# Performance work log

Measured on AMD Instinct MI355X. Metric: run time of the kernel, lower is better.

## Reference

```python
import jax, jax.numpy as jnp
import numpy as np

B, S, HID = 2, 1024, 2048
NH, NKV = 32, 8
HD = HID // NH          # 64
N_REP = NH // NKV       # 4
ROPE_BASE = 10000.0


def rope_tables(seq_len, dim):
    inv_freq = 1.0 / (ROPE_BASE ** (np.arange(0, dim, 2, dtype=np.float32) / dim))
    t = jnp.arange(seq_len, dtype=jnp.float32)
    freqs = jnp.outer(t, jnp.asarray(inv_freq))          # [S, HD/2]
    emb = jnp.concatenate([freqs, freqs], axis=-1)       # [S, HD]
    return jnp.cos(emb), jnp.sin(emb)


def rotate_half(x):
    half = x.shape[-1] // 2
    return jnp.concatenate([-x[..., half:], x[..., :half]], axis=-1)


def setup_inputs() -> dict:
    key = jax.random.key(0)
    k1, k2, k3, k4, k5 = jax.random.split(key, 5)
    hidden_states = jax.random.normal(k1, (B, S, HID), dtype=jnp.float32)
    position_ids = jnp.broadcast_to(jnp.arange(S, dtype=jnp.int32), (B, S))
    # additive causal mask [B,1,S,S]: 0 where allowed, large negative where masked
    neg = jnp.finfo(jnp.float32).min
    causal = jnp.tril(jnp.ones((S, S), dtype=bool))
    attention_mask = jnp.where(causal, 0.0, neg)[None, None].astype(jnp.float32)
    attention_mask = jnp.broadcast_to(attention_mask, (B, 1, S, S))
    scale = 0.02
    Wq = jax.random.normal(k2, (HID, NH * HD), dtype=jnp.float32) * scale
    Wk = jax.random.normal(k3, (HID, NKV * HD), dtype=jnp.float32) * scale
    Wv = jax.random.normal(k4, (HID, NKV * HD), dtype=jnp.float32) * scale
    Wo = jax.random.normal(k5, (HID, HID), dtype=jnp.float32) * scale
    return {"hidden_states": hidden_states, "position_ids": position_ids,
            "attention_mask": attention_mask, "Wq": Wq, "Wk": Wk, "Wv": Wv, "Wo": Wo}


def reference(hidden_states, position_ids, attention_mask, Wq, Wk, Wv, Wo):
    b, s, _ = hidden_states.shape
    q = (hidden_states @ Wq).reshape(b, s, NH, HD).transpose(0, 2, 1, 3)    # [b,H,s,d]
    k = (hidden_states @ Wk).reshape(b, s, NKV, HD).transpose(0, 2, 1, 3)   # [b,kv,s,d]
    v = (hidden_states @ Wv).reshape(b, s, NKV, HD).transpose(0, 2, 1, 3)

    cos_t, sin_t = rope_tables(s, HD)                    # [s, d]
    cos = cos_t[position_ids][:, None]                   # [b,1,s,d]
    sin = sin_t[position_ids][:, None]
    q = q * cos + rotate_half(q) * sin
    k = k * cos + rotate_half(k) * sin

    # GQA: repeat each kv head N_REP times along the head axis
    k = jnp.repeat(k, N_REP, axis=1)                     # [b,H,s,d]
    v = jnp.repeat(v, N_REP, axis=1)

    scale = 1.0 / jnp.sqrt(jnp.asarray(HD, dtype=q.dtype))
    scores = jnp.einsum('bhqd,bhkd->bhqk', q, k) * scale
    scores = scores + attention_mask
    scores = jnp.maximum(scores, jnp.finfo(scores.dtype).min)
    w = jax.nn.softmax(scores, axis=-1)
    out = jnp.einsum('bhqk,bhkd->bhqd', w, v)            # [b,H,s,d]
    out = out.transpose(0, 2, 1, 3).reshape(b, s, HID)
    return out @ Wo
```

## Files before the change

kernel.cpp:

```cpp
#include <hip/hip_runtime.h>
#include <hip/hip_bf16.h>
#include <math.h>

constexpr int BB   = 2;
constexpr int SS   = 1024;
constexpr int HID  = 2048;
constexpr int NH   = 32;
constexpr int NKV  = 8;
constexpr int HD   = 64;
constexpr int M    = BB * SS;
constexpr int NQKV = 3072;

typedef __attribute__((ext_vector_type(8))) short bf8v;
typedef __attribute__((ext_vector_type(4))) float f4v;

static __device__ __forceinline__ unsigned short f2b(float x) {
  __hip_bfloat16 h = __float2bfloat16(x);
  return *reinterpret_cast<unsigned short*>(&h);
}
static __device__ __forceinline__ void gload16(void* lds, const void* g) {
  __builtin_amdgcn_global_load_lds(
      (const __attribute__((address_space(1))) void*)g,
      (__attribute__((address_space(3))) void*)lds, 16, 0, 0);
}

__global__ __launch_bounds__(256) void prepAll(
    const float* __restrict__ Wq, const float* __restrict__ Wk,
    const float* __restrict__ Wv, const float* __restrict__ Wo,
    const float* __restrict__ hidden, const int* __restrict__ pos_ids,
    unsigned short* __restrict__ WqkvT, unsigned short* __restrict__ WoT,
    unsigned short* __restrict__ Xb, float2* __restrict__ tab) {
  const int z = blockIdx.z;
  const int t = threadIdx.x;

  if (z == 4) {
    const int idx = blockIdx.y * 32 + blockIdx.x;
    if ((t & 127) < 32) {
      const int m = idx * 2 + (t >> 7);
      const int j = t & 31;
      const float pos = (float)pos_ids[m];
      const float ang = pos * exp2f(-(float)j * (13.287712379549449f / 32.0f));
      float sn, cs;
      sincosf(ang, &sn, &cs);
      tab[(size_t)m * 32 + j] = make_float2(cs, sn);
    }
    return;
  }
  if (z == 5) {
    const size_t base = ((size_t)(blockIdx.y * 32 + blockIdx.x)) * 4096;
#pragma unroll
    for (int it = 0; it < 2; ++it) {
      const size_t i = base + it * 2048 + t * 8;
      const float4 v0 = *(const float4*)(hidden + i);
      const float4 v1 = *(const float4*)(hidden + i + 4);
      unsigned short o[8] = {f2b(v0.x), f2b(v0.y), f2b(v0.z), f2b(v0.w),
                             f2b(v1.x), f2b(v1.y), f2b(v1.z), f2b(v1.w)};
      *(bf8v*)(Xb + i) = *(bf8v*)o;
    }
    return;
  }

  const float* src;
  unsigned short* dst;
  int C;
  if (z == 0)      { src = Wq; dst = WqkvT;                      C = 2048; }
  else if (z == 1) { src = Wk; dst = WqkvT + (size_t)2048 * HID; C = 512;  }
  else if (z == 2) { src = Wv; dst = WqkvT + (size_t)2560 * HID; C = 512;  }
  else             { src = Wo; dst = WoT;                        C = 2048; }

  const int r0 = blockIdx.y * 64, c0 = blockIdx.x * 64;
  if (c0 >= C) return;
  __shared__ float T[64][65];
  {
    const int r  = t >> 2;
    const int c4 = (t & 3) * 16;
    const float* sp = src + (size_t)(r0 + r) * C + c0 + c4;
    *(float4*)&T[r][c4 + 0]  = *(const float4*)(sp + 0);
    *(float4*)&T[r][c4 + 4]  = *(const float4*)(sp + 4);
    *(float4*)&T[r][c4 + 8]  = *(const float4*)(sp + 8);
    *(float4*)&T[r][c4 + 12] = *(const float4*)(sp + 12);
  }
  __syncthreads();
  {
    const int c  = t >> 2;
    const int rr = (t & 3) * 16;
    unsigned short o[16];
#pragma unroll
    for (int i = 0; i < 16; ++i) o[i] = f2b(T[rr + i][c]);
    unsigned short* dp = dst + (size_t)(c0 + c) * HID + r0 + rr;
    *(bf8v*)dp       = *(bf8v*)&o[0];
    *(bf8v*)(dp + 8) = *(bf8v*)&o[8];
  }
}


__global__ __launch_bounds__(256) void gemm_qkv(
    const unsigned short* __restrict__ A, const unsigned short* __restrict__ Bt,
    const float2* __restrict__ tab,
    unsigned short* __restrict__ Qb, unsigned short* __restrict__ Kb,
    unsigned short* __restrict__ Vt) {
  __shared__ unsigned short As[4][64 * 32];
  __shared__ unsigned short Bs[4][128 * 32];
  const int t  = threadIdx.x;
  const int w  = t >> 6, l = t & 63;
  const int lr = l & 15, lg = l >> 4;
  const int wr = w >> 1, wc = w & 1;
  const int bm = blockIdx.y * 64, bn = blockIdx.x * 128;

  f4v acc[2][4] = {};

  const unsigned short* Ablk = A  + (size_t)bm * HID;
  const unsigned short* Bblk = Bt + (size_t)bn * HID;
  const int srow = l >> 2;
  const int scol = (((l & 3) ^ ((srow >> 1) & 3)) * 8);
  const int rsl  = (lg ^ ((lr >> 1) & 3)) * 8;

  auto stage = [&](int buf, int k0) {
    gload16(&As[buf][(w * 16) * 32], Ablk + (size_t)(w * 16 + srow) * HID + k0 + scol);
    gload16(&Bs[buf][(w * 32)      * 32], Bblk + (size_t)(w * 32 +      srow) * HID + k0 + scol);
    gload16(&Bs[buf][(w * 32 + 16) * 32], Bblk + (size_t)(w * 32 + 16 + srow) * HID + k0 + scol);
  };

  const int nsteps = HID / 32;
  stage(0, 0);
  stage(1, 32);
  stage(2, 64);
  asm volatile("s_waitcnt vmcnt(6)" ::: "memory");
  __builtin_amdgcn_s_barrier();

  const int aoff = (wr * 32 + lr) * 32 + rsl;
  const int boff = (wc * 64 + lr) * 32 + rsl;
  for (int tt = 0; tt < nsteps; ++tt) {
    const int cur = tt & 3;
    if (tt + 3 < nsteps) stage((tt + 3) & 3, (tt + 3) * 32);

    bf8v aF[2], bF[4];
#pragma unroll
    for (int i = 0; i < 2; ++i)
      aF[i] = *(const bf8v*)&As[cur][aoff + i * 512];
#pragma unroll
    for (int j = 0; j < 4; ++j)
      bF[j] = *(const bf8v*)&Bs[cur][boff + j * 512];
    __builtin_amdgcn_s_setprio(1);
#pragma unroll
    for (int mi = 0; mi < 2; ++mi)
#pragma unroll
      for (int ni = 0; ni < 4; ++ni)
        acc[mi][ni] = __builtin_amdgcn_mfma_f32_16x16x32_bf16(aF[mi], bF[ni], acc[mi][ni], 0, 0, 0);
    __builtin_amdgcn_s_setprio(0);

    if (tt + 3 < nsteps)      { asm volatile("s_waitcnt vmcnt(6)" ::: "memory"); }
    else if (tt + 2 < nsteps) { asm volatile("s_waitcnt vmcnt(3)" ::: "memory"); }
    else                      { asm volatile("s_waitcnt vmcnt(0)" ::: "memory"); }
    __builtin_amdgcn_s_barrier();
  }

  const int row0 = bm + wr * 32;
  const int colHead = bn + wc * 64;
  int mode, hh;
  if (colHead < 2048)      { mode = 0; hh = colHead >> 6;          }
  else if (colHead < 2560) { mode = 1; hh = (colHead - 2048) >> 6; }
  else                     { mode = 2; hh = (colHead - 2560) >> 6; }

#pragma unroll
  for (int mi = 0; mi < 2; ++mi)
#pragma unroll
    for (int r = 0; r < 4; ++r) {
      const int rowg = row0 + mi * 16 + lg * 4 + r;
      const int bI = rowg >> 10, s = rowg & (SS - 1);
      if (mode == 2) {
        unsigned short* base = Vt + ((size_t)(bI * NKV + hh) * 64) * SS + s;
#pragma unroll
        for (int ni = 0; ni < 4; ++ni)
          base[(size_t)(ni * 16 + lr) * SS] = f2b(acc[mi][ni][r]);
      } else {
        unsigned short* dst = (mode == 0)
            ? Qb + ((size_t)(bI * NH  + hh) * SS + s) * 64
            : Kb + ((size_t)(bI * NKV + hh) * SS + s) * 64;
        const float2 cs_lo = tab[(size_t)rowg * 32 + lr];
        const float2 cs_hi = tab[(size_t)rowg * 32 + 16 + lr];
#pragma unroll
        for (int ni = 0; ni < 4; ++ni) {
          const float2 cs = (ni & 1) ? cs_hi : cs_lo;
          const float x   = acc[mi][ni][r];
          const float prt = acc[mi][ni ^ 2][r];
          const float rh  = (ni < 2) ? -prt : prt;
          float v = x * cs.x + rh * cs.y;
          if (mode == 0) v *= 0.125f;
          dst[ni * 16 + lr] = f2b(v);
        }
      }
    }
}

__global__ __launch_bounds__(256) void gemm_bf16(
    const unsigned short* __restrict__ A, const unsigned short* __restrict__ Bt,
    float* __restrict__ C, int Ndim) {
  __shared__ unsigned short As[4][64 * 32];
  __shared__ unsigned short Bs[4][128 * 32];
  const int t  = threadIdx.x;
  const int w  = t >> 6, l = t & 63;
  const int lr = l & 15, lg = l >> 4;
  const int wr = w >> 1, wc = w & 1;
  const int bm = blockIdx.y * 64, bn = blockIdx.x * 128;

  f4v acc[2][4] = {};

  const unsigned short* Ablk = A  + (size_t)bm * HID;
  const unsigned short* Bblk = Bt + (size_t)bn * HID;
  const int srow = l >> 2;
  const int scol = (((l & 3) ^ ((srow >> 1) & 3)) * 8);
  const int rsl  = (lg ^ ((lr >> 1) & 3)) * 8;

  auto stage = [&](int buf, int k0) {
    gload16(&As[buf][(w * 16) * 32], Ablk + (size_t)(w * 16 + srow) * HID + k0 + scol);
    gload16(&Bs[buf][(w * 32)      * 32], Bblk + (size_t)(w * 32 +      srow) * HID + k0 + scol);
    gload16(&Bs[buf][(w * 32 + 16) * 32], Bblk + (size_t)(w * 32 + 16 + srow) * HID + k0 + scol);
  };

  const int nsteps = HID / 32;
  stage(0, 0);
  stage(1, 32);
  stage(2, 64);
  asm volatile("s_waitcnt vmcnt(6)" ::: "memory");
  __builtin_amdgcn_s_barrier();

  const int aoff = (wr * 32 + lr) * 32 + rsl;
  const int boff = (wc * 64 + lr) * 32 + rsl;
  for (int tt = 0; tt < nsteps; ++tt) {
    const int cur = tt & 3;
    if (tt + 3 < nsteps) stage((tt + 3) & 3, (tt + 3) * 32);

    bf8v aF[2], bF[4];
#pragma unroll
    for (int i = 0; i < 2; ++i)
      aF[i] = *(const bf8v*)&As[cur][aoff + i * 512];
#pragma unroll
    for (int j = 0; j < 4; ++j)
      bF[j] = *(const bf8v*)&Bs[cur][boff + j * 512];
    __builtin_amdgcn_s_setprio(1);
#pragma unroll
    for (int mi = 0; mi < 2; ++mi)
#pragma unroll
      for (int ni = 0; ni < 4; ++ni)
        acc[mi][ni] = __builtin_amdgcn_mfma_f32_16x16x32_bf16(aF[mi], bF[ni], acc[mi][ni], 0, 0, 0);
    __builtin_amdgcn_s_setprio(0);

    if (tt + 3 < nsteps)      { asm volatile("s_waitcnt vmcnt(6)" ::: "memory"); }
    else if (tt + 2 < nsteps) { asm volatile("s_waitcnt vmcnt(3)" ::: "memory"); }
    else                      { asm volatile("s_waitcnt vmcnt(0)" ::: "memory"); }
    __builtin_amdgcn_s_barrier();
  }

  const int row0 = bm + wr * 32;
  const int col0 = bn + wc * 64;
#pragma unroll
  for (int mi = 0; mi < 2; ++mi)
#pragma unroll
    for (int r = 0; r < 4; ++r) {
      const size_t rowoff = (size_t)(row0 + mi * 16 + lg * 4 + r) * Ndim;
#pragma unroll
      for (int ni = 0; ni < 4; ++ni)
        C[rowoff + col0 + ni * 16 + lr] = acc[mi][ni][r];
    }
}

__global__ __launch_bounds__(128) void attn_mfma(
    const unsigned short* __restrict__ Qb, const unsigned short* __restrict__ Kb,
    const unsigned short* __restrict__ Vt, unsigned short* __restrict__ attn) {
  const int xb = blockIdx.x;
  const int h = blockIdx.y, b = blockIdx.z;
  const int kv = h >> 2;
  const int w  = threadIdx.x >> 6;
  const int l  = threadIdx.x & 63;
  const int lr = l & 15;
  const int lg = l >> 4;
  const int t  = threadIdx.x;

  __shared__ unsigned short VT[64][72];
  __shared__ unsigned short PL[2][16][72];

  const unsigned short* Kp = Kb + ((size_t)((b * NKV + kv) * SS)) * 64;
  const unsigned short* Vp = Vt + ((size_t)((b * NKV + kv) * 64)) * SS;

  const int vd  = t >> 1;
  const int vso = (t & 1) * 32;

  for (int half = 0; half < 2; ++half) {
    const int qt = half ? (31 - xb) : xb;
    const int qbase = qt * 32;
    const int qW = qbase + w * 16;
    const unsigned short* Qp = Qb + ((size_t)((b * NH + h) * SS + qW)) * 64;
    bf8v aQ0 = *(const bf8v*)(Qp + (size_t)lr * 64 + lg * 8);
    bf8v aQ1 = *(const bf8v*)(Qp + (size_t)lr * 64 + 32 + lg * 8);

    f4v o[4] = {{0,0,0,0},{0,0,0,0},{0,0,0,0},{0,0,0,0}};
    float lsumL[4] = {0.f, 0.f, 0.f, 0.f};

    bf8v kc[8];
#pragma unroll
    for (int c = 0; c < 4; ++c) {
      const unsigned short* kr = Kp + (size_t)(c * 16 + lr) * 64 + lg * 8;
      kc[2 * c]     = *(const bf8v*)(kr);
      kc[2 * c + 1] = *(const bf8v*)(kr + 32);
    }

    for (int kvb = 0; kvb < qbase + 32; kvb += 64) {
      __syncthreads();
      const unsigned short* vp = Vp + (size_t)vd * SS + kvb + vso;
      const bf8v v0 = *(const bf8v*)(vp);
      const bf8v v1 = *(const bf8v*)(vp + 8);
      const bf8v v2 = *(const bf8v*)(vp + 16);
      const bf8v v3 = *(const bf8v*)(vp + 24);

      f4v sc[4] = {{0,0,0,0},{0,0,0,0},{0,0,0,0},{0,0,0,0}};
      __builtin_amdgcn_s_setprio(1);
#pragma unroll
      for (int c = 0; c < 4; ++c) {
        sc[c] = __builtin_amdgcn_mfma_f32_16x16x32_bf16(aQ0, kc[2 * c],     sc[c], 0, 0, 0);
        sc[c] = __builtin_amdgcn_mfma_f32_16x16x32_bf16(aQ1, kc[2 * c + 1], sc[c], 0, 0, 0);
      }
      __builtin_amdgcn_s_setprio(0);

      if (kvb + 64 < qbase + 32) {
#pragma unroll
        for (int c = 0; c < 4; ++c) {
          const unsigned short* kr = Kp + (size_t)(kvb + 64 + c * 16 + lr) * 64 + lg * 8;
          kc[2 * c]     = *(const bf8v*)(kr);
          kc[2 * c + 1] = *(const bf8v*)(kr + 32);
        }
      }

#pragma unroll
      for (int r = 0; r < 4; ++r) {
        const int qrow = qW + lg * 4 + r;
        float ps = 0.f;
        unsigned short pb[4];
#pragma unroll
        for (int c = 0; c < 4; ++c) {
          const float s = ((kvb + c * 16 + lr) > qrow) ? -INFINITY : sc[c][r];
          const float p = __expf(s);
          ps += p;
          pb[c] = f2b(p);
        }
        lsumL[r] += ps;
#pragma unroll
        for (int c = 0; c < 4; ++c) PL[w][lg * 4 + r][c * 16 + lr] = pb[c];
      }

      *(bf8v*)&VT[vd][vso]      = v0;
      *(bf8v*)&VT[vd][vso + 8]  = v1;
      *(bf8v*)&VT[vd][vso + 16] = v2;
      *(bf8v*)&VT[vd][vso + 24] = v3;

      __syncthreads();

      bf8v aP0 = *(const bf8v*)&PL[w][lr][lg * 8];
      bf8v aP1 = *(const bf8v*)&PL[w][lr][32 + lg * 8];
      __builtin_amdgcn_s_setprio(1);
#pragma unroll
      for (int n = 0; n < 4; ++n) {
        bf8v bV0 = *(const bf8v*)&VT[n * 16 + lr][lg * 8];
        bf8v bV1 = *(const bf8v*)&VT[n * 16 + lr][32 + lg * 8];
        o[n] = __builtin_amdgcn_mfma_f32_16x16x32_bf16(aP0, bV0, o[n], 0, 0, 0);
        o[n] = __builtin_amdgcn_mfma_f32_16x16x32_bf16(aP1, bV1, o[n], 0, 0, 0);
      }
      __builtin_amdgcn_s_setprio(0);
    }

#pragma unroll
    for (int r = 0; r < 4; ++r) {
      float ls = lsumL[r];
      ls += __shfl_xor(ls, 1);
      ls += __shfl_xor(ls, 2);
      ls += __shfl_xor(ls, 4);
      ls += __shfl_xor(ls, 8);
      const float inv = 1.0f / ls;
      const int row = qW + lg * 4 + r;
      unsigned short* dst = attn + (size_t)(b * SS + row) * HID + h * 64;
#pragma unroll
      for (int n = 0; n < 4; ++n) dst[n * 16 + lr] = f2b(o[n][r] * inv);
    }
  }
}

extern "C" void kernel_launch(void* const* d_in, const int* in_sizes, int n_in,
                              void* d_out, int out_size, void* d_ws, size_t ws_size,
                              hipStream_t stream) {
  const float* hidden = (const float*)d_in[0];
  const int*   pos    = (const int*)d_in[1];
  const float* Wq = (const float*)d_in[3];
  const float* Wk = (const float*)d_in[4];
  const float* Wv = (const float*)d_in[5];
  const float* Wo = (const float*)d_in[6];
  float* out = (float*)d_out;

  char* ws = (char*)d_ws;
  unsigned short* WqkvT = (unsigned short*)(ws);
  unsigned short* WoT   = (unsigned short*)(ws + 12582912);
  unsigned short* Xb    = (unsigned short*)(ws + 20971520);
  unsigned short* attnb = Xb;
  unsigned short* Qb    = (unsigned short*)(ws + 29360128);
  unsigned short* Kb    = (unsigned short*)(ws + 37748736);
  unsigned short* Vt    = (unsigned short*)(ws + 39845888);
  float2*         tab   = (float2*)(ws + 41943040);

  dim3 blk(256);

  prepAll<<<dim3(32, 32, 6), blk, 0, stream>>>(Wq, Wk, Wv, Wo, hidden, pos,
                                               WqkvT, WoT, Xb, tab);

  gemm_qkv<<<dim3(NQKV / 128, M / 64), blk, 0, stream>>>(Xb, WqkvT, tab, Qb, Kb, Vt);

  attn_mfma<<<dim3(16, NH, BB), dim3(128), 0, stream>>>(Qb, Kb, Vt, attnb);

  gemm_bf16<<<dim3(HID / 128, M / 64), blk, 0, stream>>>(attnb, WoT, out, HID);
}
```

Before: 149.1 us.

## Use 8 waves per GEMM block with one 16-row tile per wave

Both bf16 GEMMs now launch 512 threads (8 waves) per 64x128 block instead of 4. Each wave computes a 16x64 sub-tile rather than 32x64, and the LDS staging is split so waves 0-3 load A and B rows while waves 4-7 load only B rows, with per-wave vmcnt waits. The aim is more wavefronts to hide latency, at the cost of halving per-wave MFMA work against the same LDS B-fragment reads and adding barrier overhead.

Result: no change. 148.5 us (-0.4%).

```diff
diff --git a/kernel.cpp b/kernel.cpp
--- a/kernel.cpp
+++ b/kernel.cpp
@@ -94,7 +94,7 @@
 }
 
 
-__global__ __launch_bounds__(256) void gemm_qkv(
+__global__ __launch_bounds__(512) void gemm_qkv(
     const unsigned short* __restrict__ A, const unsigned short* __restrict__ Bt,
     const float2* __restrict__ tab,
     unsigned short* __restrict__ Qb, unsigned short* __restrict__ Kb,
@@ -107,7 +107,7 @@
   const int wr = w >> 1, wc = w & 1;
   const int bm = blockIdx.y * 64, bn = blockIdx.x * 128;
 
-  f4v acc[2][4] = {};
+  f4v acc[4] = {};
 
   const unsigned short* Ablk = A  + (size_t)bm * HID;
   const unsigned short* Bblk = Bt + (size_t)bn * HID;
@@ -116,46 +116,52 @@
   const int rsl  = (lg ^ ((lr >> 1) & 3)) * 8;
 
   auto stage = [&](int buf, int k0) {
-    gload16(&As[buf][(w * 16) * 32], Ablk + (size_t)(w * 16 + srow) * HID + k0 + scol);
-    gload16(&Bs[buf][(w * 32)      * 32], Bblk + (size_t)(w * 32 +      srow) * HID + k0 + scol);
-    gload16(&Bs[buf][(w * 32 + 16) * 32], Bblk + (size_t)(w * 32 + 16 + srow) * HID + k0 + scol);
+    if (w < 4) {
+      gload16(&As[buf][(w * 16) * 32], Ablk + (size_t)(w * 16 + srow) * HID + k0 + scol);
+      gload16(&Bs[buf][(w * 16) * 32], Bblk + (size_t)(w * 16 + srow) * HID + k0 + scol);
+    } else {
+      gload16(&Bs[buf][(w * 16) * 32], Bblk + (size_t)(w * 16 + srow) * HID + k0 + scol);
+    }
   };
 
   const int nsteps = HID / 32;
   stage(0, 0);
   stage(1, 32);
   stage(2, 64);
-  asm volatile("s_waitcnt vmcnt(6)" ::: "memory");
+  if (w < 4) { asm volatile("s_waitcnt vmcnt(4)" ::: "memory"); }
+  else       { asm volatile("s_waitcnt vmcnt(2)" ::: "memory"); }
   __builtin_amdgcn_s_barrier();
 
-  const int aoff = (wr * 32 + lr) * 32 + rsl;
+  const int aoff = (wr * 16 + lr) * 32 + rsl;
   const int boff = (wc * 64 + lr) * 32 + rsl;
   for (int tt = 0; tt < nsteps; ++tt) {
     const int cur = tt & 3;
     if (tt + 3 < nsteps) stage((tt + 3) & 3, (tt + 3) * 32);
 
-    bf8v aF[2], bF[4];
-#pragma unroll
-    for (int i = 0; i < 2; ++i)
-      aF[i] = *(const bf8v*)&As[cur][aoff + i * 512];
+    bf8v aF = *(const bf8v*)&As[cur][aoff];
+    bf8v bF[4];
 #pragma unroll
     for (int j = 0; j < 4; ++j)
       bF[j] = *(const bf8v*)&Bs[cur][boff + j * 512];
     __builtin_amdgcn_s_setprio(1);
 #pragma unroll
-    for (int mi = 0; mi < 2; ++mi)
-#pragma unroll
-      for (int ni = 0; ni < 4; ++ni)
-        acc[mi][ni] = __builtin_amdgcn_mfma_f32_16x16x32_bf16(aF[mi], bF[ni], acc[mi][ni], 0, 0, 0);
+    for (int ni = 0; ni < 4; ++ni)
+      acc[ni] = __builtin_amdgcn_mfma_f32_16x16x32_bf16(aF, bF[ni], acc[ni], 0, 0, 0);
     __builtin_amdgcn_s_setprio(0);
 
-    if (tt + 3 < nsteps)      { asm volatile("s_waitcnt vmcnt(6)" ::: "memory"); }
-    else if (tt + 2 < nsteps) { asm volatile("s_waitcnt vmcnt(3)" ::: "memory"); }
-    else                      { asm volatile("s_waitcnt vmcnt(0)" ::: "memory"); }
+    if (tt + 3 < nsteps) {
+      if (w < 4) { asm volatile("s_waitcnt vmcnt(4)" ::: "memory"); }
+      else       { asm volatile("s_waitcnt vmcnt(2)" ::: "memory"); }
+    } else if (tt + 2 < nsteps) {
+      if (w < 4) { asm volatile("s_waitcnt vmcnt(2)" ::: "memory"); }
+      else       { asm volatile("s_waitcnt vmcnt(1)" ::: "memory"); }
+    } else {
+      asm volatile("s_waitcnt vmcnt(0)" ::: "memory");
+    }
     __builtin_amdgcn_s_barrier();
   }
 
-  const int row0 = bm + wr * 32;
+  const int row0 = bm + wr * 16;
   const int colHead = bn + wc * 64;
   int mode, hh;
   if (colHead < 2048)      { mode = 0; hh = colHead >> 6;          }
@@ -163,37 +169,35 @@
   else                     { mode = 2; hh = (colHead - 2560) >> 6; }
 
 #pragma unroll
-  for (int mi = 0; mi < 2; ++mi)
-#pragma unroll
-    for (int r = 0; r < 4; ++r) {
-      const int rowg = row0 + mi * 16 + lg * 4 + r;
-      const int bI = rowg >> 10, s = rowg & (SS - 1);
-      if (mode == 2) {
-        unsigned short* base = Vt + ((size_t)(bI * NKV + hh) * 64) * SS + s;
-#pragma unroll
-        for (int ni = 0; ni < 4; ++ni)
-          base[(size_t)(ni * 16 + lr) * SS] = f2b(acc[mi][ni][r]);
-      } else {
-        unsigned short* dst = (mode == 0)
-            ? Qb + ((size_t)(bI * NH  + hh) * SS + s) * 64
-            : Kb + ((size_t)(bI * NKV + hh) * SS + s) * 64;
-        const float2 cs_lo = tab[(size_t)rowg * 32 + lr];
-        const float2 cs_hi = tab[(size_t)rowg * 32 + 16 + lr];
-#pragma unroll
-        for (int ni = 0; ni < 4; ++ni) {
-          const float2 cs = (ni & 1) ? cs_hi : cs_lo;
-          const float x   = acc[mi][ni][r];
-          const float prt = acc[mi][ni ^ 2][r];
-          const float rh  = (ni < 2) ? -prt : prt;
-          float v = x * cs.x + rh * cs.y;
-          if (mode == 0) v *= 0.125f;
-          dst[ni * 16 + lr] = f2b(v);
-        }
+  for (int r = 0; r < 4; ++r) {
+    const int rowg = row0 + lg * 4 + r;
+    const int bI = rowg >> 10, s = rowg & (SS - 1);
+    if (mode == 2) {
+      unsigned short* base = Vt + ((size_t)(bI * NKV + hh) * 64) * SS + s;
+#pragma unroll
+      for (int ni = 0; ni < 4; ++ni)
+        base[(size_t)(ni * 16 + lr) * SS] = f2b(acc[ni][r]);
+    } else {
+      unsigned short* dst = (mode == 0)
+          ? Qb + ((size_t)(bI * NH  + hh) * SS + s) * 64
+          : Kb + ((size_t)(bI * NKV + hh) * SS + s) * 64;
+      const float2 cs_lo = tab[(size_t)rowg * 32 + lr];
+      const float2 cs_hi = tab[(size_t)rowg * 32 + 16 + lr];
+#pragma unroll
+      for (int ni = 0; ni < 4; ++ni) {
+        const float2 cs = (ni & 1) ? cs_hi : cs_lo;
+        const float x   = acc[ni][r];
+        const float prt = acc[ni ^ 2][r];
+        const float rh  = (ni < 2) ? -prt : prt;
+        float v = x * cs.x + rh * cs.y;
+        if (mode == 0) v *= 0.125f;
+        dst[ni * 16 + lr] = f2b(v);
       }
     }
-}
-
-__global__ __launch_bounds__(256) void gemm_bf16(
+  }
+}
+
+__global__ __launch_bounds__(512) void gemm_bf16(
     const unsigned short* __restrict__ A, const unsigned short* __restrict__ Bt,
     float* __restrict__ C, int Ndim) {
   __shared__ unsigned short As[4][64 * 32];
@@ -204,7 +208,7 @@
   const int wr = w >> 1, wc = w & 1;
   const int bm = blockIdx.y * 64, bn = blockIdx.x * 128;
 
-  f4v acc[2][4] = {};
+  f4v acc[4] = {};
 
   const unsigned short* Ablk = A  + (size_t)bm * HID;
   const unsigned short* Bblk = Bt + (size_t)bn * HID;
@@ -213,56 +217,60 @@
   const int rsl  = (lg ^ ((lr >> 1) & 3)) * 8;
 
   auto stage = [&](int buf, int k0) {
-    gload16(&As[buf][(w * 16) * 32], Ablk + (size_t)(w * 16 + srow) * HID + k0 + scol);
-    gload16(&Bs[buf][(w * 32)      * 32], Bblk + (size_t)(w * 32 +      srow) * HID + k0 + scol);
-    gload16(&Bs[buf][(w * 32 + 16) * 32], Bblk + (size_t)(w * 32 + 16 + srow) * HID + k0 + scol);
+    if (w < 4) {
+      gload16(&As[buf][(w * 16) * 32], Ablk + (size_t)(w * 16 + srow) * HID + k0 + scol);
+      gload16(&Bs[buf][(w * 16) * 32], Bblk + (size_t)(w * 16 + srow) * HID + k0 + scol);
+    } else {
+      gload16(&Bs[buf][(w * 16) * 32], Bblk + (size_t)(w * 16 + srow) * HID + k0 + scol);
+    }
   };
 
   const int nsteps = HID / 32;
   stage(0, 0);
   stage(1, 32);
   stage(2, 64);
-  asm volatile("s_waitcnt vmcnt(6)" ::: "memory");
+  if (w < 4) { asm volatile("s_waitcnt vmcnt(4)" ::: "memory"); }
+  else       { asm volatile("s_waitcnt vmcnt(2)" ::: "memory"); }
   __builtin_amdgcn_s_barrier();
 
-  const int aoff = (wr * 32 + lr) * 32 + rsl;
+  const int aoff = (wr * 16 + lr) * 32 + rsl;
   const int boff = (wc * 64 + lr) * 32 + rsl;
   for (int tt = 0; tt < nsteps; ++tt) {
     const int cur = tt & 3;
     if (tt + 3 < nsteps) stage((tt + 3) & 3, (tt + 3) * 32);
 
-    bf8v aF[2], bF[4];
-#pragma unroll
-    for (int i = 0; i < 2; ++i)
-      aF[i] = *(const bf8v*)&As[cur][aoff + i * 512];
+    bf8v aF = *(const bf8v*)&As[cur][aoff];
+    bf8v bF[4];
 #pragma unroll
     for (int j = 0; j < 4; ++j)
       bF[j] = *(const bf8v*)&Bs[cur][boff + j * 512];
     __builtin_amdgcn_s_setprio(1);
 #pragma unroll
-    for (int mi = 0; mi < 2; ++mi)
-#pragma unroll
-      for (int ni = 0; ni < 4; ++ni)
-        acc[mi][ni] = __builtin_amdgcn_mfma_f32_16x16x32_bf16(aF[mi], bF[ni], acc[mi][ni], 0, 0, 0);
+    for (int ni = 0; ni < 4; ++ni)
+      acc[ni] = __builtin_amdgcn_mfma_f32_16x16x32_bf16(aF, bF[ni], acc[ni], 0, 0, 0);
     __builtin_amdgcn_s_setprio(0);
 
-    if (tt + 3 < nsteps)      { asm volatile("s_waitcnt vmcnt(6)" ::: "memory"); }
-    else if (tt + 2 < nsteps) { asm volatile("s_waitcnt vmcnt(3)" ::: "memory"); }
-    else                      { asm volatile("s_waitcnt vmcnt(0)" ::: "memory"); }
+    if (tt + 3 < nsteps) {
+      if (w < 4) { asm volatile("s_waitcnt vmcnt(4)" ::: "memory"); }
+      else       { asm volatile("s_waitcnt vmcnt(2)" ::: "memory"); }
+    } else if (tt + 2 < nsteps) {
+      if (w < 4) { asm volatile("s_waitcnt vmcnt(2)" ::: "memory"); }
+      else       { asm volatile("s_waitcnt vmcnt(1)" ::: "memory"); }
+    } else {
+      asm volatile("s_waitcnt vmcnt(0)" ::: "memory");
+    }
     __builtin_amdgcn_s_barrier();
   }
 
-  const int row0 = bm + wr * 32;
+  const int row0 = bm + wr * 16;
   const int col0 = bn + wc * 64;
 #pragma unroll
-  for (int mi = 0; mi < 2; ++mi)
-#pragma unroll
-    for (int r = 0; r < 4; ++r) {
-      const size_t rowoff = (size_t)(row0 + mi * 16 + lg * 4 + r) * Ndim;
-#pragma unroll
-      for (int ni = 0; ni < 4; ++ni)
-        C[rowoff + col0 + ni * 16 + lr] = acc[mi][ni][r];
-    }
+  for (int r = 0; r < 4; ++r) {
+    const size_t rowoff = (size_t)(row0 + lg * 4 + r) * Ndim;
+#pragma unroll
+    for (int ni = 0; ni < 4; ++ni)
+      C[rowoff + col0 + ni * 16 + lr] = acc[ni][r];
+  }
 }
 
 __global__ __launch_bounds__(128) void attn_mfma(
@@ -410,9 +418,9 @@
   prepAll<<<dim3(32, 32, 6), blk, 0, stream>>>(Wq, Wk, Wv, Wo, hidden, pos,
                                                WqkvT, WoT, Xb, tab);
 
-  gemm_qkv<<<dim3(NQKV / 128, M / 64), blk, 0, stream>>>(Xb, WqkvT, tab, Qb, Kb, Vt);
+  gemm_qkv<<<dim3(NQKV / 128, M / 64), dim3(512), 0, stream>>>(Xb, WqkvT, tab, Qb, Kb, Vt);
 
   attn_mfma<<<dim3(16, NH, BB), dim3(128), 0, stream>>>(Qb, Kb, Vt, attnb);
 
-  gemm_bf16<<<dim3(HID / 128, M / 64), blk, 0, stream>>>(attnb, WoT, out, HID);
-}
+  gemm_bf16<<<dim3(HID / 128, M / 64), dim3(512), 0, stream>>>(attnb, WoT, out, HID);
+}
```
